# Performance work log

Hardware: AMD Instinct MI355X
Metric: run time of the kernel (lower is better)

## Reference

```python
import jax, jax.numpy as jnp
import numpy as np

H = 16            # num_heads
SEG = 2048        # segment_size
DIL = 8           # dilation_rate
BLOCK_M = 64      # triton query block size (min(64, M_padded))


def setup_inputs() -> dict:
    key = jax.random.key(0)
    k1, k2, k3 = jax.random.split(key, 3)
    B, M, D = 2, 8192, 1024
    x = jax.random.normal(k1, (B, M, D), dtype=jnp.float32)
    Wqkv = jax.random.normal(k2, (3 * D, D), dtype=jnp.float32) * 0.02
    Wout = jax.random.normal(k3, (D, D), dtype=jnp.float32) * 0.02
    return {"x": x, "Wqkv": Wqkv, "Wout": Wout}


def reference(x, Wqkv, Wout):
    B, M, D = x.shape
    hd = D // H
    scale = hd ** -0.5
    S = M // SEG                      # number of segments (M is a multiple of SEG)
    Kn = SEG // DIL                   # dilated keys per segment
    nb = SEG // BLOCK_M               # query blocks per segment

    # qkv projection (torch Linear: x @ W^T), split into q,k,v: [B,H,M,hd]
    qkv = jnp.einsum('bmd,ed->bme', x, Wqkv).reshape(B, M, 3, H, hd)
    qkv = jnp.transpose(qkv, (2, 0, 3, 1, 4))
    q, k, v = qkv[0] * scale, qkv[1], qkv[2]

    # segment-local views
    q4 = q.reshape(B, H, S, SEG, hd)
    k4 = k.reshape(B, H, S, SEG, hd)[:, :, :, ::DIL]   # [B,H,S,Kn,hd] dilated keys
    v4 = v.reshape(B, H, S, SEG, hd)[:, :, :, ::DIL]

    # scores per segment: [B,H,S,SEG,Kn]
    scores = jnp.einsum('bhspd,bhskd->bhspk', q4, k4)
    # kernel normalization: per key j, subtract max over the 64-query block
    scores = scores.reshape(B, H, S, nb, BLOCK_M, Kn)
    c = jnp.max(scores, axis=4, keepdims=True)          # [B,H,S,nb,1,Kn]
    w = jnp.exp(scores - c)
    den = jnp.sum(w, axis=-1) + 1e-10                   # [B,H,S,nb,BLOCK_M]
    num = jnp.einsum('bhsnmk,bhskd->bhsnmd', w, v4)
    out = num / den[..., None]                          # [B,H,S,nb,BLOCK_M,hd]

    out = out.reshape(B, H, M, hd)
    out = jnp.transpose(out, (0, 2, 1, 3)).reshape(B, M, D)
    return jnp.einsum('bmd,ed->bme', out, Wout)
```

## Files before the change

kernel.cpp:

```cpp
#include <hip/hip_runtime.h>
#include <hip/hip_bf16.h>
#include <stdint.h>


typedef __attribute__((ext_vector_type(8))) short short8;
typedef __attribute__((ext_vector_type(4))) float f32x4;
typedef __attribute__((ext_vector_type(4))) unsigned short ushort4v;

#define DEVI static __device__ __forceinline__

DEVI unsigned short f2bf(float f) {
  union { float f; uint32_t u; } v; v.f = f;
  return (unsigned short)((v.u + 0x7FFFu + ((v.u >> 16) & 1u)) >> 16);
}

DEVI void gload_lds16(const void* g, void* l) {
  __builtin_amdgcn_global_load_lds((const __attribute__((address_space(1))) void*)g,
                                   (__attribute__((address_space(3))) void*)l,
                                   16, 0, 0);
}

__global__ void cvt_kernel(const float* __restrict__ in, unsigned short* __restrict__ out, int n) {
  int i = (blockIdx.x * 256 + threadIdx.x) * 4;
  if (i >= n) return;
  float4 f = *(const float4*)(in + i);
  uint2 o;
  o.x = (uint32_t)f2bf(f.x) | ((uint32_t)f2bf(f.y) << 16);
  o.y = (uint32_t)f2bf(f.z) | ((uint32_t)f2bf(f.w) << 16);
  *(uint2*)(out + i) = o;
}

template<int EPI>
__global__ __launch_bounds__(256, 2) void gemm_bt(
    const unsigned short* __restrict__ A, const unsigned short* __restrict__ B,
    void* __restrict__ Cv, unsigned short* __restrict__ Cv2,
    float scale, long a_row_stride, int ldc, int K)
{
  __shared__ unsigned short smA[128 * 64];
  __shared__ unsigned short smB[128 * 64];
  const int tid = threadIdx.x;
  const int tm = blockIdx.x, tn = blockIdx.y;
  const int w = tid >> 6, lane = tid & 63;
  const int wr = (w >> 1) * 64, wc = (w & 1) * 64;
  const int lr = lane & 15, lq = lane >> 4;

  int se[4], srow[4], scol[4];
#pragma unroll
  for (int i = 0; i < 4; ++i) {
    int e = (i * 256 + tid) * 8;
    int r = e >> 6;
    int cc = (e >> 3) & 7;
    se[i] = e; srow[i] = r; scol[i] = (cc ^ (r & 7)) * 8;
  }

  f32x4 acc[4][4] = {};

  for (int kt = 0; kt < K / 64; ++kt) {
    if (kt) __syncthreads();
#pragma unroll
    for (int i = 0; i < 4; ++i)
      gload_lds16(A + (long)(tm * 128 + srow[i]) * a_row_stride + kt * 64 + scol[i], &smA[se[i]]);
#pragma unroll
    for (int i = 0; i < 4; ++i)
      gload_lds16(B + (long)(tn * 128 + srow[i]) * K + kt * 64 + scol[i], &smB[se[i]]);
    __syncthreads();

#pragma unroll
    for (int kk = 0; kk < 2; ++kk) {
      int kc = kk * 4 + lq;
      short8 af[4], bfm[4];
#pragma unroll
      for (int i = 0; i < 4; ++i) {
        int row = wr + i * 16 + lr;
        af[i] = *(const short8*)&smA[row * 64 + ((kc ^ (row & 7)) * 8)];
      }
#pragma unroll
      for (int j = 0; j < 4; ++j) {
        int row = wc + j * 16 + lr;
        bfm[j] = *(const short8*)&smB[row * 64 + ((kc ^ (row & 7)) * 8)];
      }
#pragma unroll
      for (int i = 0; i < 4; ++i)
#pragma unroll
        for (int j = 0; j < 4; ++j)
          acc[i][j] = __builtin_amdgcn_mfma_f32_16x16x32_bf16(af[i], bfm[j], acc[i][j], 0, 0, 0);
    }
  }

  if (EPI == 2 && tn >= 8) {
#pragma unroll
    for (int i = 0; i < 4; ++i) {
      int m0 = tm * 128 + wr + i * 16 + lq * 4;
      long rowbase = (long)(m0 >> 8) * 1024;
#pragma unroll
      for (int j = 0; j < 4; ++j) {
        int f = (tn - 8) * 128 + wc + j * 16 + lr;
        ushort4v p;
#pragma unroll
        for (int r = 0; r < 4; ++r) p[r] = f2bf(acc[i][j][r] * scale);
        *(ushort4v*)&Cv2[(rowbase + f) * 256 + (m0 & 255)] = p;
      }
    }
    return;
  }

#pragma unroll
  for (int i = 0; i < 4; ++i) {
    int rg0 = tm * 128 + wr + i * 16 + lq * 4;
#pragma unroll
    for (int j = 0; j < 4; ++j) {
      int cg = tn * 128 + wc + j * 16 + lr;
#pragma unroll
      for (int r = 0; r < 4; ++r) {
        float v = acc[i][j][r] * scale;
        long off = (long)(rg0 + r) * ldc + cg;
        if (EPI == 0) ((float*)Cv)[off] = v;
        else          ((unsigned short*)Cv)[off] = f2bf(v);
      }
    }
  }
}

__global__ __launch_bounds__(256, 2) void attn_kernel(
    const unsigned short* __restrict__ qb,
    const unsigned short* __restrict__ kb,
    const unsigned short* __restrict__ vtb,
    unsigned short* __restrict__ attout)
{
  __shared__ unsigned short k_t[256 * 64];
  __shared__ unsigned short v_t[64 * 256];
  __shared__ unsigned short w_lds[64 * 128];

  const int bid = blockIdx.x;
  const int quarter = bid & 3, s = (bid >> 2) & 3, h = (bid >> 4) & 15, b = bid >> 8;
  const int tid = threadIdx.x, w = tid >> 6, lane = tid & 63;
  const int lr = lane & 15, lq = lane >> 4;
  const long qrow0 = (long)b * 8192 + s * 2048 + quarter * 512;
  const int hc = h * 64;

  const unsigned short* kbase = kb + ((long)(b * 4 + s) * 256) * 1024 + hc;
  const unsigned short* vbase = vtb + ((long)(b * 4 + s) * 1024 + hc) * 256;

#pragma unroll
  for (int it = 0; it < 8; ++it) {
    int e = (it * 256 + tid) * 8;
    int row = e >> 6;
    int ch = (e >> 3) & 7;
    gload_lds16(kbase + (long)row * 1024 + ((ch ^ (row & 7)) * 8), &k_t[e]);
  }
#pragma unroll
  for (int it = 0; it < 8; ++it) {
    int e = (it * 256 + tid) * 8;
    int f = e >> 8;
    int ch = (e >> 3) & 31;
    gload_lds16(vbase + (long)f * 256 + ((ch ^ (f & 7)) * 8), &v_t[e]);
  }
  __syncthreads();

  short8 ones;
#pragma unroll
  for (int e = 0; e < 8; ++e) ones[e] = (short)0x3F80;

  for (int qblk = 0; qblk < 8; ++qblk) {
    const unsigned short* qbase = qb + (qrow0 + qblk * 64) * 1024 + hc;
    f32x4 acc_pv[4] = {};
    f32x4 acc_den = {};

#pragma unroll
    for (int half = 0; half < 2; ++half) {
      f32x4 acc_s[4][2] = {};
#pragma unroll
      for (int kk = 0; kk < 2; ++kk) {
        int kc = kk * 4 + lq;
        short8 aq[4], bk[2];
#pragma unroll
        for (int i = 0; i < 4; ++i)
          aq[i] = *(const short8*)&qbase[(i * 16 + lr) * 1024 + kc * 8];
#pragma unroll
        for (int j = 0; j < 2; ++j) {
          int row = half * 128 + w * 32 + j * 16 + lr;
          bk[j] = *(const short8*)&k_t[row * 64 + ((kc ^ (row & 7)) * 8)];
        }
#pragma unroll
        for (int i = 0; i < 4; ++i)
#pragma unroll
          for (int j = 0; j < 2; ++j)
            acc_s[i][j] = __builtin_amdgcn_mfma_f32_16x16x32_bf16(aq[i], bk[j], acc_s[i][j], 0, 0, 0);
      }

      float cmax[2];
#pragma unroll
      for (int j = 0; j < 2; ++j) {
        float m = -3.4e38f;
#pragma unroll
        for (int i = 0; i < 4; ++i)
#pragma unroll
          for (int r = 0; r < 4; ++r) m = fmaxf(m, acc_s[i][j][r]);
        m = fmaxf(m, __shfl_xor(m, 16));
        m = fmaxf(m, __shfl_xor(m, 32));
        cmax[j] = m;
      }

#pragma unroll
      for (int i = 0; i < 4; ++i) {
#pragma unroll
        for (int r = 0; r < 4; ++r) {
          int q = i * 16 + lq * 4 + r;
#pragma unroll
          for (int jf = 0; jf < 2; ++jf) {
            int col = w * 32 + jf * 16 + lr;
            float wv = __expf(acc_s[i][jf][r] - cmax[jf]);
            w_lds[q * 128 + ((((col >> 3) ^ (q & 7)) << 3) | (col & 7))] = f2bf(wv);
          }
        }
      }
      __syncthreads();

#pragma unroll
      for (int ks = 0; ks < 4; ++ks) {
        int kc = ks * 4 + lq;
        int qrow = w * 16 + lr;
        short8 bw = *(const short8*)&w_lds[qrow * 128 + ((kc ^ (lr & 7)) << 3)];
        acc_den = __builtin_amdgcn_mfma_f32_16x16x32_bf16(ones, bw, acc_den, 0, 0, 0);
#pragma unroll
        for (int ct = 0; ct < 4; ++ct) {
          int frow = ct * 16 + lr;
          short8 av = *(const short8*)&v_t[frow * 256 + (((half * 16 + kc) ^ (lr & 7)) << 3)];
          acc_pv[ct] = __builtin_amdgcn_mfma_f32_16x16x32_bf16(av, bw, acc_pv[ct], 0, 0, 0);
        }
      }
      __syncthreads();
    }

    float inv = 1.0f / (acc_den[0] + 1e-10f);
    long orow = (qrow0 + qblk * 64 + w * 16 + lr) * 1024 + hc;
#pragma unroll
    for (int ct = 0; ct < 4; ++ct) {
      ushort4v p;
#pragma unroll
      for (int r = 0; r < 4; ++r) p[r] = f2bf(acc_pv[ct][r] * inv);
      *(ushort4v*)&attout[orow + ct * 16 + lq * 4] = p;
    }
  }
}

extern "C" void kernel_launch(void* const* d_in, const int* in_sizes, int n_in,
                              void* d_out, int out_size, void* d_ws, size_t ws_size,
                              hipStream_t stream) {
  (void)in_sizes; (void)n_in; (void)out_size; (void)ws_size;
  const float* x    = (const float*)d_in[0];
  const float* Wqkv = (const float*)d_in[1];
  const float* Wout = (const float*)d_in[2];
  float* out = (float*)d_out;
  char* ws = (char*)d_ws;

  unsigned short* xb     = (unsigned short*)(ws);
  unsigned short* attout = (unsigned short*)(ws);
  unsigned short* wqkvb  = (unsigned short*)(ws + 33554432);
  unsigned short* woutb  = (unsigned short*)(ws + 39845888);
  unsigned short* qbuf   = (unsigned short*)(ws + 41943040);
  unsigned short* kbuf   = (unsigned short*)(ws + 75497472);
  unsigned short* vtb    = (unsigned short*)(ws + 79691776);

  cvt_kernel<<<16384, 256, 0, stream>>>(x, xb, 16777216);
  cvt_kernel<<<3072, 256, 0, stream>>>(Wqkv, wqkvb, 3 * 1024 * 1024);
  cvt_kernel<<<1024, 256, 0, stream>>>(Wout, woutb, 1024 * 1024);

  gemm_bt<1><<<dim3(128, 8), 256, 0, stream>>>(
      xb, wqkvb, (void*)qbuf, nullptr, 0.125f, 1024, 1024, 1024);
  gemm_bt<2><<<dim3(16, 16), 256, 0, stream>>>(
      xb, wqkvb + 1024 * 1024, (void*)kbuf, vtb, 1.0f, 8192, 1024, 1024);

  attn_kernel<<<512, 256, 0, stream>>>(qbuf, kbuf, vtb, attout);

  gemm_bt<0><<<dim3(128, 8), 256, 0, stream>>>(
      attout, woutb, (void*)out, nullptr, 1.0f, 1024, 1024, 1024);
}
```

Baseline: 201.0 us.

## Keep K fragments in registers and double attention grid with interleaved key order

The attention kernel drops the K tile from LDS and holds each wave's K fragments in registers, shrinks the W buffer to a padded packed-uint32 layout, and splits each segment into eight query chunks so the grid doubles to 1024 blocks at occupancy 3. To make this consistent, the V-transposed epilogue of the K/V GEMM stores an interleaved key ordering that matches the packed W columns, with 16-byte stores. The aim is less LDS traffic and footprint plus more parallelism. In exchange, K is reloaded by twice as many blocks and register pressure rises.

```diff
diff --git a/kernel.cpp b/kernel.cpp
--- a/kernel.cpp
+++ b/kernel.cpp
@@ -12,6 +12,10 @@
 DEVI unsigned short f2bf(float f) {
   union { float f; uint32_t u; } v; v.f = f;
   return (unsigned short)((v.u + 0x7FFFu + ((v.u >> 16) & 1u)) >> 16);
+}
+
+DEVI uint32_t pack_bf16(float lo, float hi) {
+  return (uint32_t)f2bf(lo) | ((uint32_t)f2bf(hi) << 16);
 }
 
 DEVI void gload_lds16(const void* g, void* l) {
@@ -88,17 +92,23 @@
   }
 
   if (EPI == 2 && tn >= 8) {
-#pragma unroll
-    for (int i = 0; i < 4; ++i) {
-      int m0 = tm * 128 + wr + i * 16 + lq * 4;
-      long rowbase = (long)(m0 >> 8) * 1024;
+    const int fbase = (tn - 8) * 128 + wc;
+#pragma unroll
+    for (int ip = 0; ip < 4; ip += 2) {
+      int t0 = tm * 128 + wr + ip * 16 + lq * 4;
+      int seg = t0 >> 8;
+      int ts  = t0 & 255;
+      int c32 = (ts >> 5) * 16 + (ts & 15);
 #pragma unroll
       for (int j = 0; j < 4; ++j) {
-        int f = (tn - 8) * 128 + wc + j * 16 + lr;
-        ushort4v p;
-#pragma unroll
-        for (int r = 0; r < 4; ++r) p[r] = f2bf(acc[i][j][r] * scale);
-        *(ushort4v*)&Cv2[(rowbase + f) * 256 + (m0 & 255)] = p;
+        int f = fbase + j * 16 + lr;
+        uint32_t* rp = (uint32_t*)&Cv2[((long)(seg * 1024 + f)) * 256];
+        uint4 U;
+        U.x = pack_bf16(acc[ip][j][0] * scale, acc[ip + 1][j][0] * scale);
+        U.y = pack_bf16(acc[ip][j][1] * scale, acc[ip + 1][j][1] * scale);
+        U.z = pack_bf16(acc[ip][j][2] * scale, acc[ip + 1][j][2] * scale);
+        U.w = pack_bf16(acc[ip][j][3] * scale, acc[ip + 1][j][3] * scale);
+        *(uint4*)&rp[c32] = U;
       }
     }
     return;
@@ -121,33 +131,25 @@
   }
 }
 
-__global__ __launch_bounds__(256, 2) void attn_kernel(
+__global__ __launch_bounds__(256, 3) void attn_kernel(
     const unsigned short* __restrict__ qb,
     const unsigned short* __restrict__ kb,
     const unsigned short* __restrict__ vtb,
     unsigned short* __restrict__ attout)
 {
-  __shared__ unsigned short k_t[256 * 64];
   __shared__ unsigned short v_t[64 * 256];
-  __shared__ unsigned short w_lds[64 * 128];
-
-  const int bid = blockIdx.x;
-  const int quarter = bid & 3, s = (bid >> 2) & 3, h = (bid >> 4) & 15, b = bid >> 8;
+  __shared__ uint32_t w32[64 * 68];
+
+  const int u = (blockIdx.x & 7) * 128 + (blockIdx.x >> 3);
+  const int e8 = u & 7, h = (u >> 3) & 15, s = (u >> 7) & 3, b = u >> 9;
   const int tid = threadIdx.x, w = tid >> 6, lane = tid & 63;
   const int lr = lane & 15, lq = lane >> 4;
-  const long qrow0 = (long)b * 8192 + s * 2048 + quarter * 512;
+  const long qrow0 = (long)b * 8192 + s * 2048 + e8 * 256;
   const int hc = h * 64;
 
   const unsigned short* kbase = kb + ((long)(b * 4 + s) * 256) * 1024 + hc;
   const unsigned short* vbase = vtb + ((long)(b * 4 + s) * 1024 + hc) * 256;
 
-#pragma unroll
-  for (int it = 0; it < 8; ++it) {
-    int e = (it * 256 + tid) * 8;
-    int row = e >> 6;
-    int ch = (e >> 3) & 7;
-    gload_lds16(kbase + (long)row * 1024 + ((ch ^ (row & 7)) * 8), &k_t[e]);
-  }
 #pragma unroll
   for (int it = 0; it < 8; ++it) {
     int e = (it * 256 + tid) * 8;
@@ -155,13 +157,24 @@
     int ch = (e >> 3) & 31;
     gload_lds16(vbase + (long)f * 256 + ((ch ^ (f & 7)) * 8), &v_t[e]);
   }
+
+  short8 bk[2][2][2];
+#pragma unroll
+  for (int half = 0; half < 2; ++half)
+#pragma unroll
+    for (int kk = 0; kk < 2; ++kk)
+#pragma unroll
+      for (int jf = 0; jf < 2; ++jf)
+        bk[half][kk][jf] = *(const short8*)
+          &kbase[(long)(half * 128 + w * 32 + jf * 16 + lr) * 1024 + (kk * 4 + lq) * 8];
+
   __syncthreads();
 
   short8 ones;
 #pragma unroll
   for (int e = 0; e < 8; ++e) ones[e] = (short)0x3F80;
 
-  for (int qblk = 0; qblk < 8; ++qblk) {
+  for (int qblk = 0; qblk < 4; ++qblk) {
     const unsigned short* qbase = qb + (qrow0 + qblk * 64) * 1024 + hc;
     f32x4 acc_pv[4] = {};
     f32x4 acc_den = {};
@@ -172,20 +185,15 @@
 #pragma unroll
       for (int kk = 0; kk < 2; ++kk) {
         int kc = kk * 4 + lq;
-        short8 aq[4], bk[2];
+        short8 aq[4];
 #pragma unroll
         for (int i = 0; i < 4; ++i)
           aq[i] = *(const short8*)&qbase[(i * 16 + lr) * 1024 + kc * 8];
 #pragma unroll
-        for (int j = 0; j < 2; ++j) {
-          int row = half * 128 + w * 32 + j * 16 + lr;
-          bk[j] = *(const short8*)&k_t[row * 64 + ((kc ^ (row & 7)) * 8)];
-        }
-#pragma unroll
         for (int i = 0; i < 4; ++i)
 #pragma unroll
           for (int j = 0; j < 2; ++j)
-            acc_s[i][j] = __builtin_amdgcn_mfma_f32_16x16x32_bf16(aq[i], bk[j], acc_s[i][j], 0, 0, 0);
+            acc_s[i][j] = __builtin_amdgcn_mfma_f32_16x16x32_bf16(aq[i], bk[half][kk][j], acc_s[i][j], 0, 0, 0);
       }
 
       float cmax[2];
@@ -206,12 +214,9 @@
 #pragma unroll
         for (int r = 0; r < 4; ++r) {
           int q = i * 16 + lq * 4 + r;
-#pragma unroll
-          for (int jf = 0; jf < 2; ++jf) {
-            int col = w * 32 + jf * 16 + lr;
-            float wv = __expf(acc_s[i][jf][r] - cmax[jf]);
-            w_lds[q * 128 + ((((col >> 3) ^ (q & 7)) << 3) | (col & 7))] = f2bf(wv);
-          }
+          uint32_t pk = pack_bf16(__expf(acc_s[i][0][r] - cmax[0]),
+                                  __expf(acc_s[i][1][r] - cmax[1]));
+          w32[q * 68 + w * 16 + lr] = pk;
         }
       }
       __syncthreads();
@@ -219,8 +224,7 @@
 #pragma unroll
       for (int ks = 0; ks < 4; ++ks) {
         int kc = ks * 4 + lq;
-        int qrow = w * 16 + lr;
-        short8 bw = *(const short8*)&w_lds[qrow * 128 + ((kc ^ (lr & 7)) << 3)];
+        short8 bw = *(const short8*)&w32[(w * 16 + lr) * 68 + kc * 4];
         acc_den = __builtin_amdgcn_mfma_f32_16x16x32_bf16(ones, bw, acc_den, 0, 0, 0);
 #pragma unroll
         for (int ct = 0; ct < 4; ++ct) {
@@ -271,7 +275,7 @@
   gemm_bt<2><<<dim3(16, 16), 256, 0, stream>>>(
       xb, wqkvb + 1024 * 1024, (void*)kbuf, vtb, 1.0f, 8192, 1024, 1024);
 
-  attn_kernel<<<512, 256, 0, stream>>>(qbuf, kbuf, vtb, attout);
+  attn_kernel<<<1024, 256, 0, stream>>>(qbuf, kbuf, vtb, attout);
 
   gemm_bt<0><<<dim3(128, 8), 256, 0, stream>>>(
       attout, woutb, (void*)out, nullptr, 1.0f, 1024, 1024, 1024);
```

Result: no change. 198.2 us (-1.4%).
